# Performance work log

Hardware: AMD Instinct MI355X
Metric: run time of the kernel (lower is better)

The kernel has to match this reference:

```python
import jax, jax.numpy as jnp
import numpy as np

N = 50000   # num nodes
D = 64      # feature dim
R = 4       # num relations (len(adjs))
E = 800000  # edges per relation (avg degree 16)


def setup_inputs() -> dict:
    key = jax.random.key(0)
    k0, k1, k2, k3, k4 = jax.random.split(key, 5)
    x = jax.random.normal(k0, (N, D), dtype=jnp.float32)
    weight = jax.random.normal(k1, (R,), dtype=jnp.float32)        # scalar weight per relation
    edge_vals = jax.random.uniform(k2, (R, E), dtype=jnp.float32)  # nonzero values of adjs
    edge_rows = jax.random.randint(k3, (R, E), 0, N)               # COO row (destination) indices
    edge_cols = jax.random.randint(k4, (R, E), 0, N)               # COO col (source) indices
    return {"x": x, "weight": weight, "edge_vals": edge_vals,
            "edge_rows": edge_rows, "edge_cols": edge_cols, "idx": 1}


def reference(x, weight, edge_vals, edge_rows, edge_cols, idx):
    # spmm(adjs[idx], x): gather source features, scale by edge values, scatter-add to rows
    rows = edge_rows[idx]
    cols = edge_cols[idx]
    vals = edge_vals[idx]
    msgs = vals[:, None] * x[cols]                                  # [E, D]
    agg = jax.ops.segment_sum(msgs, rows, num_segments=N)           # [N, D]
    return weight[idx] * agg
```

## Files before the change

kernel.cpp:

```cpp
#include <hip/hip_runtime.h>


#define FEAT_D 64
#define BROWS 32
#define BSH 5
#define LCAP 48
#define OVFCAP 16384
#define EPB 4096
#define BBLOCK 512
#define EPT (EPB / BBLOCK)
#define GBLOCK 512

__global__ __launch_bounds__(BBLOCK) void build_kernel(
        const float* __restrict__ edge_vals,
        const int* __restrict__ edge_rows,
        const int* __restrict__ edge_cols,
        const int* __restrict__ idx_ptr,
        int* __restrict__ bktcnt,
        int2* __restrict__ pack,
        int* __restrict__ ovfcnt,
        int4* __restrict__ ovfbuf,
        int E, int NBKT, int cap) {
    extern __shared__ int lh[];
    const long long off = (long long)idx_ptr[0] * E;
    const int* rows = edge_rows + off;
    const int* cols = edge_cols + off;
    const float* vals = edge_vals + off;
    for (int k = threadIdx.x; k < NBKT; k += BBLOCK) lh[k] = 0;
    __syncthreads();
    const int s = blockIdx.x * EPB;
    const int e2 = min(s + EPB, E);
    int myrow[EPT];
#pragma unroll
    for (int k = 0; k < EPT; ++k) {
        const int g = s + threadIdx.x + k * BBLOCK;
        if (g < e2) {
            const int r = rows[g];
            myrow[k] = r;
            atomicAdd(&lh[r >> BSH], 1);
        }
    }
    __syncthreads();
    for (int k = threadIdx.x; k < NBKT; k += BBLOCK) {
        const int c = lh[k];
        if (c) lh[k] = atomicAdd(&bktcnt[k], c);
    }
    __syncthreads();
#pragma unroll
    for (int k = 0; k < EPT; ++k) {
        const int g = s + threadIdx.x + k * BBLOCK;
        if (g < e2) {
            const int r = myrow[k];
            const int b = r >> BSH;
            const int c = cols[g];
            const float v = vals[g];
            const int pos = atomicAdd(&lh[b], 1);
            if (pos < cap) {
                pack[(long long)b * cap + pos] =
                    make_int2((c << BSH) | (r & (BROWS - 1)), __float_as_int(v));
            } else {
                const int o = atomicAdd(ovfcnt, 1);
                if (o < OVFCAP) ovfbuf[o] = make_int4(r, c, __float_as_int(v), 0);
            }
        }
    }
}

__global__ __launch_bounds__(GBLOCK) void gather_kernel(
        const float* __restrict__ x,
        const float* __restrict__ weight,
        const int* __restrict__ idx_ptr,
        const int* __restrict__ bktcnt,
        const int2* __restrict__ pack,
        int* __restrict__ ovfcnt, int4* __restrict__ ovfbuf,
        float* __restrict__ out, int N, int cap) {
    __shared__ int2 slist[BROWS * LCAP];
    __shared__ int scur[BROWS];
    const int b = blockIdx.x;
    const int t = threadIdx.x;
    const int w = t >> 6;
    const int lane = t & 63;
    if (t < BROWS) scur[t] = 0;
    __syncthreads();
    const int cnt = min(bktcnt[b], cap);
    const long long* psrc = (const long long*)(pack + (long long)b * cap);
    for (int j = t; j < cnt; j += GBLOCK) {
        const long long raw = __builtin_nontemporal_load(psrc + j);
        const int2 rec = make_int2((int)(unsigned)raw, (int)(raw >> 32));
        const int rl = rec.x & (BROWS - 1);
        const int li = atomicAdd(&scur[rl], 1);
        if (li < LCAP) {
            slist[rl * LCAP + li] = rec;
        } else {
            const int o = atomicAdd(ovfcnt, 1);
            const int row = (b << BSH) | rl;
            if (o < OVFCAP) ovfbuf[o] = make_int4(row, rec.x >> BSH, rec.y, 0);
        }
    }
    __syncthreads();
    const float ws = weight[idx_ptr[0]];
    float acc0 = 0.f, acc1 = 0.f, acc2 = 0.f, acc3 = 0.f;
#define ROWACC(Q, ACC)                                                        \
    {                                                                         \
        const int rl = w * 4 + Q;                                             \
        const int n = min(scur[rl], LCAP);                                    \
        const int2* lp = slist + rl * LCAP;                                   \
        int j = 0;                                                            \
        for (; j + 4 <= n; j += 4) {                                          \
            const int2 r0 = lp[j], r1 = lp[j + 1], r2 = lp[j + 2],            \
                       r3 = lp[j + 3];                                        \
            const float x0 = x[(r0.x >> BSH) * FEAT_D + lane];                \
            const float x1 = x[(r1.x >> BSH) * FEAT_D + lane];                \
            const float x2 = x[(r2.x >> BSH) * FEAT_D + lane];                \
            const float x3 = x[(r3.x >> BSH) * FEAT_D + lane];                \
            ACC += __int_as_float(r0.y) * x0 + __int_as_float(r1.y) * x1 +    \
                   __int_as_float(r2.y) * x2 + __int_as_float(r3.y) * x3;     \
        }                                                                     \
        for (; j < n; ++j) {                                                  \
            const int2 r0 = lp[j];                                            \
            ACC += __int_as_float(r0.y) * x[(r0.x >> BSH) * FEAT_D + lane];   \
        }                                                                     \
    }
    ROWACC(0, acc0)
    ROWACC(1, acc1)
    ROWACC(2, acc2)
    ROWACC(3, acc3)
#undef ROWACC
    const int row0 = (b << BSH) + w * 4;
    if (row0 + 0 < N)
        __builtin_nontemporal_store(ws * acc0, &out[(long long)(row0 + 0) * FEAT_D + lane]);
    if (row0 + 1 < N)
        __builtin_nontemporal_store(ws * acc1, &out[(long long)(row0 + 1) * FEAT_D + lane]);
    if (row0 + 2 < N)
        __builtin_nontemporal_store(ws * acc2, &out[(long long)(row0 + 2) * FEAT_D + lane]);
    if (row0 + 3 < N)
        __builtin_nontemporal_store(ws * acc3, &out[(long long)(row0 + 3) * FEAT_D + lane]);
}

__global__ void fixup_kernel(const float* __restrict__ x,
                             const float* __restrict__ weight,
                             const int* __restrict__ idx_ptr,
                             const int* __restrict__ ovfcnt,
                             const int4* __restrict__ ovfbuf,
                             float* __restrict__ out) {
    const int n = min(*ovfcnt, OVFCAP);
    if (n == 0) return;
    const float ws = weight[idx_ptr[0]];
    const int gw = (int)((blockIdx.x * (long long)blockDim.x + threadIdx.x) >> 6);
    const int lane = threadIdx.x & 63;
    const int nw = (gridDim.x * blockDim.x) >> 6;
    for (int r = gw; r < n; r += nw) {
        const int4 rec = ovfbuf[r];
        atomicAdd(&out[(long long)rec.x * FEAT_D + lane],
                  ws * __int_as_float(rec.z) * x[(long long)rec.y * FEAT_D + lane]);
    }
}

__global__ void spmm_scatter_kernel(const float* __restrict__ x,
                                    const float* __restrict__ weight,
                                    const float* __restrict__ edge_vals,
                                    const int* __restrict__ edge_rows,
                                    const int* __restrict__ edge_cols,
                                    const int* __restrict__ idx_ptr,
                                    float* __restrict__ out,
                                    int E, long long work) {
    const int idx = idx_ptr[0];
    const float w = weight[idx];
    const long long rel_off = (long long)idx * E;
    long long t = (long long)blockIdx.x * blockDim.x + threadIdx.x;
    if (t >= work) return;
    const int e = (int)(t >> 4);
    const int q = (int)(t & 15);
    const int r = edge_rows[rel_off + e];
    const int c = edge_cols[rel_off + e];
    const float wv = w * edge_vals[rel_off + e];
    const float4 xv = *reinterpret_cast<const float4*>(x + (long long)c * FEAT_D + q * 4);
    float* op = out + (long long)r * FEAT_D + q * 4;
    atomicAdd(op + 0, wv * xv.x);
    atomicAdd(op + 1, wv * xv.y);
    atomicAdd(op + 2, wv * xv.z);
    atomicAdd(op + 3, wv * xv.w);
}

extern "C" void kernel_launch(void* const* d_in, const int* in_sizes, int n_in,
                              void* d_out, int out_size, void* d_ws, size_t ws_size,
                              hipStream_t stream) {
    const float* x         = (const float*)d_in[0];
    const float* weight    = (const float*)d_in[1];
    const float* edge_vals = (const float*)d_in[2];
    const int*   edge_rows = (const int*)d_in[3];
    const int*   edge_cols = (const int*)d_in[4];
    const int*   idx_ptr   = (const int*)d_in[5];
    float* out = (float*)d_out;

    const int R = in_sizes[1];
    const int E = in_sizes[2] / R;
    const int N = in_sizes[0] / FEAT_D;
    const int NBKT = (N + BROWS - 1) >> BSH;

    char* ws = (char*)d_ws;
    size_t o_bktcnt = 0;
    size_t o_ovfcnt = o_bktcnt + (size_t)NBKT * 4;
    size_t o_ovfbuf = ((o_ovfcnt + 4 + 15) / 16) * 16;
    size_t o_pack   = o_ovfbuf + (size_t)OVFCAP * 16;
    const size_t room = (ws_size > o_pack) ? (ws_size - o_pack) : 0;
    int cap = (int)(room / ((size_t)NBKT * 8));
    if (cap > 1024) cap = 1024;

    const long long meanload = (NBKT > 0) ? ((long long)E / NBKT) : 0;
    if (cap < 64 || cap < meanload + (meanload >> 3) + 16 || NBKT > 8192) {
        hipMemsetAsync(d_out, 0, (size_t)out_size * sizeof(float), stream);
        const long long work = (long long)E * 16;
        const int block = 256;
        const long long grid = (work + block - 1) / block;
        spmm_scatter_kernel<<<dim3((unsigned)grid), dim3(block), 0, stream>>>(
            x, weight, edge_vals, edge_rows, edge_cols, idx_ptr, out, E, work);
        return;
    }

    int*  bktcnt = (int*)(ws + o_bktcnt);
    int*  ovfcnt = (int*)(ws + o_ovfcnt);
    int4* ovfbuf = (int4*)(ws + o_ovfbuf);
    int2* pack   = (int2*)(ws + o_pack);

    hipMemsetAsync(bktcnt, 0, (size_t)NBKT * 4 + 4, stream);

    const int bgrid = (E + EPB - 1) / EPB;
    const size_t blds = (size_t)NBKT * 4;
    build_kernel<<<bgrid, BBLOCK, blds, stream>>>(edge_vals, edge_rows,
                                                  edge_cols, idx_ptr, bktcnt,
                                                  pack, ovfcnt, ovfbuf,
                                                  E, NBKT, cap);

    gather_kernel<<<NBKT, GBLOCK, 0, stream>>>(x, weight, idx_ptr, bktcnt,
                                               pack, ovfcnt, ovfbuf,
                                               out, N, cap);

    fixup_kernel<<<64, 256, 0, stream>>>(x, weight, idx_ptr, ovfcnt, ovfbuf, out);
}
```

Baseline: 138.8 us.

## Stage edges in LDS by bucket before coalesced global writes; widen buckets

The build kernel now counting-sorts each 4096-edge chunk by destination bucket in shared memory, using a block prefix scan, before writing. Each bucket's records can then go out as a contiguous run with one global atomic per bucket, instead of scattered per-edge writes. Buckets grow from 32 to 64 rows, so each gather wave handles 8 rows and the pack capacity and fallback thresholds are raised to match. In exchange, the build kernel uses far more static shared memory and loses occupancy, the gather grid halves, and a smaller workspace would push execution onto the slow scatter fallback.

```diff
diff --git a/kernel.cpp b/kernel.cpp
--- a/kernel.cpp
+++ b/kernel.cpp
@@ -2,9 +2,10 @@
 
 
 #define FEAT_D 64
-#define BROWS 32
-#define BSH 5
-#define LCAP 48
+#define BROWS 64
+#define BSH 6
+#define MAXBKT 1024
+#define LCAP 44
 #define OVFCAP 16384
 #define EPB 4096
 #define BBLOCK 512
@@ -21,47 +22,89 @@
         int* __restrict__ ovfcnt,
         int4* __restrict__ ovfbuf,
         int E, int NBKT, int cap) {
-    extern __shared__ int lh[];
+    __shared__ int2 stage[EPB];
+    __shared__ unsigned short sbkt[EPB];
+    __shared__ int lh[MAXBKT];
+    __shared__ int lofs[MAXBKT];
+    __shared__ int gbase[MAXBKT];
+    __shared__ int ssum[BBLOCK];
     const long long off = (long long)idx_ptr[0] * E;
     const int* rows = edge_rows + off;
     const int* cols = edge_cols + off;
     const float* vals = edge_vals + off;
-    for (int k = threadIdx.x; k < NBKT; k += BBLOCK) lh[k] = 0;
-    __syncthreads();
+    const int t = threadIdx.x;
     const int s = blockIdx.x * EPB;
     const int e2 = min(s + EPB, E);
-    int myrow[EPT];
+    const int cnt_total = e2 - s;
+
+    for (int k = t; k < NBKT; k += BBLOCK) lh[k] = 0;
+    __syncthreads();
+
+    int2 myrec[EPT];
+    int mybkt[EPT];
 #pragma unroll
     for (int k = 0; k < EPT; ++k) {
-        const int g = s + threadIdx.x + k * BBLOCK;
+        const int g = s + t + k * BBLOCK;
+        mybkt[k] = -1;
         if (g < e2) {
             const int r = rows[g];
-            myrow[k] = r;
-            atomicAdd(&lh[r >> BSH], 1);
-        }
-    }
-    __syncthreads();
-    for (int k = threadIdx.x; k < NBKT; k += BBLOCK) {
-        const int c = lh[k];
-        if (c) lh[k] = atomicAdd(&bktcnt[k], c);
-    }
-    __syncthreads();
-#pragma unroll
-    for (int k = 0; k < EPT; ++k) {
-        const int g = s + threadIdx.x + k * BBLOCK;
-        if (g < e2) {
-            const int r = myrow[k];
-            const int b = r >> BSH;
             const int c = cols[g];
             const float v = vals[g];
-            const int pos = atomicAdd(&lh[b], 1);
-            if (pos < cap) {
-                pack[(long long)b * cap + pos] =
-                    make_int2((c << BSH) | (r & (BROWS - 1)), __float_as_int(v));
-            } else {
-                const int o = atomicAdd(ovfcnt, 1);
-                if (o < OVFCAP) ovfbuf[o] = make_int4(r, c, __float_as_int(v), 0);
-            }
+            mybkt[k] = r >> BSH;
+            myrec[k] = make_int2((c << BSH) | (r & (BROWS - 1)), __float_as_int(v));
+            atomicAdd(&lh[mybkt[k]], 1);
+        }
+    }
+    __syncthreads();
+
+    const int i0 = 2 * t, i1 = 2 * t + 1;
+    const int a0 = (i0 < NBKT) ? lh[i0] : 0;
+    const int a1 = (i1 < NBKT) ? lh[i1] : 0;
+    ssum[t] = a0 + a1;
+    __syncthreads();
+    for (int d = 1; d < BBLOCK; d <<= 1) {
+        const int add = (t >= d) ? ssum[t - d] : 0;
+        __syncthreads();
+        ssum[t] += add;
+        __syncthreads();
+    }
+    const int exc = ssum[t] - (a0 + a1);
+    if (i0 < NBKT) lofs[i0] = exc;
+    if (i1 < NBKT) lofs[i1] = exc + a0;
+    __syncthreads();
+
+    for (int k = t; k < NBKT; k += BBLOCK) lh[k] = lofs[k];
+    __syncthreads();
+
+#pragma unroll
+    for (int k = 0; k < EPT; ++k) {
+        if (mybkt[k] >= 0) {
+            const int pos = atomicAdd(&lh[mybkt[k]], 1);
+            stage[pos] = myrec[k];
+            sbkt[pos] = (unsigned short)mybkt[k];
+        }
+    }
+    __syncthreads();
+
+    for (int k = t; k < NBKT; k += BBLOCK) {
+        const int c = lh[k] - lofs[k];
+        gbase[k] = (c > 0) ? atomicAdd(&bktcnt[k], c) : 0;
+    }
+    __syncthreads();
+
+    for (int p = t; p < cnt_total; p += BBLOCK) {
+        const int k = sbkt[p];
+        const int g = gbase[k] + (p - lofs[k]);
+        const int2 rec = stage[p];
+        if (g < cap) {
+            __builtin_nontemporal_store(
+                *(const long long*)&rec,
+                (long long*)(pack + (long long)k * cap + g));
+        } else {
+            const int o = atomicAdd(ovfcnt, 1);
+            if (o < OVFCAP)
+                ovfbuf[o] = make_int4((k << BSH) | (rec.x & (BROWS - 1)),
+                                      rec.x >> BSH, rec.y, 0);
         }
     }
 }
@@ -93,48 +136,43 @@
             slist[rl * LCAP + li] = rec;
         } else {
             const int o = atomicAdd(ovfcnt, 1);
-            const int row = (b << BSH) | rl;
-            if (o < OVFCAP) ovfbuf[o] = make_int4(row, rec.x >> BSH, rec.y, 0);
+            if (o < OVFCAP)
+                ovfbuf[o] = make_int4((b << BSH) | rl, rec.x >> BSH, rec.y, 0);
         }
     }
     __syncthreads();
     const float ws = weight[idx_ptr[0]];
-    float acc0 = 0.f, acc1 = 0.f, acc2 = 0.f, acc3 = 0.f;
-#define ROWACC(Q, ACC)                                                        \
-    {                                                                         \
-        const int rl = w * 4 + Q;                                             \
-        const int n = min(scur[rl], LCAP);                                    \
-        const int2* lp = slist + rl * LCAP;                                   \
-        int j = 0;                                                            \
-        for (; j + 4 <= n; j += 4) {                                          \
-            const int2 r0 = lp[j], r1 = lp[j + 1], r2 = lp[j + 2],            \
-                       r3 = lp[j + 3];                                        \
-            const float x0 = x[(r0.x >> BSH) * FEAT_D + lane];                \
-            const float x1 = x[(r1.x >> BSH) * FEAT_D + lane];                \
-            const float x2 = x[(r2.x >> BSH) * FEAT_D + lane];                \
-            const float x3 = x[(r3.x >> BSH) * FEAT_D + lane];                \
-            ACC += __int_as_float(r0.y) * x0 + __int_as_float(r1.y) * x1 +    \
-                   __int_as_float(r2.y) * x2 + __int_as_float(r3.y) * x3;     \
-        }                                                                     \
-        for (; j < n; ++j) {                                                  \
-            const int2 r0 = lp[j];                                            \
-            ACC += __int_as_float(r0.y) * x[(r0.x >> BSH) * FEAT_D + lane];   \
-        }                                                                     \
-    }
-    ROWACC(0, acc0)
-    ROWACC(1, acc1)
-    ROWACC(2, acc2)
-    ROWACC(3, acc3)
-#undef ROWACC
-    const int row0 = (b << BSH) + w * 4;
-    if (row0 + 0 < N)
-        __builtin_nontemporal_store(ws * acc0, &out[(long long)(row0 + 0) * FEAT_D + lane]);
-    if (row0 + 1 < N)
-        __builtin_nontemporal_store(ws * acc1, &out[(long long)(row0 + 1) * FEAT_D + lane]);
-    if (row0 + 2 < N)
-        __builtin_nontemporal_store(ws * acc2, &out[(long long)(row0 + 2) * FEAT_D + lane]);
-    if (row0 + 3 < N)
-        __builtin_nontemporal_store(ws * acc3, &out[(long long)(row0 + 3) * FEAT_D + lane]);
+    float acc[8];
+#pragma unroll
+    for (int q = 0; q < 8; ++q) acc[q] = 0.f;
+#pragma unroll
+    for (int q = 0; q < 8; ++q) {
+        const int rl = w * 8 + q;
+        const int n = min(scur[rl], LCAP);
+        const int2* lp = slist + rl * LCAP;
+        int j = 0;
+        for (; j + 4 <= n; j += 4) {
+            const int2 r0 = lp[j], r1 = lp[j + 1], r2 = lp[j + 2], r3 = lp[j + 3];
+            const float x0 = x[(r0.x >> BSH) * FEAT_D + lane];
+            const float x1 = x[(r1.x >> BSH) * FEAT_D + lane];
+            const float x2 = x[(r2.x >> BSH) * FEAT_D + lane];
+            const float x3 = x[(r3.x >> BSH) * FEAT_D + lane];
+            acc[q] += __int_as_float(r0.y) * x0 + __int_as_float(r1.y) * x1 +
+                      __int_as_float(r2.y) * x2 + __int_as_float(r3.y) * x3;
+        }
+        for (; j < n; ++j) {
+            const int2 r0 = lp[j];
+            acc[q] += __int_as_float(r0.y) * x[(r0.x >> BSH) * FEAT_D + lane];
+        }
+    }
+    const int row0 = (b << BSH) + w * 8;
+#pragma unroll
+    for (int q = 0; q < 8; ++q) {
+        const int row = row0 + q;
+        if (row < N)
+            __builtin_nontemporal_store(ws * acc[q],
+                                        &out[(long long)row * FEAT_D + lane]);
+    }
 }
 
 __global__ void fixup_kernel(const float* __restrict__ x,
@@ -205,10 +243,10 @@
     size_t o_pack   = o_ovfbuf + (size_t)OVFCAP * 16;
     const size_t room = (ws_size > o_pack) ? (ws_size - o_pack) : 0;
     int cap = (int)(room / ((size_t)NBKT * 8));
-    if (cap > 1024) cap = 1024;
+    if (cap > 2048) cap = 2048;
 
     const long long meanload = (NBKT > 0) ? ((long long)E / NBKT) : 0;
-    if (cap < 64 || cap < meanload + (meanload >> 3) + 16 || NBKT > 8192) {
+    if (cap < 128 || cap < meanload + (meanload >> 3) + 32 || NBKT > MAXBKT) {
         hipMemsetAsync(d_out, 0, (size_t)out_size * sizeof(float), stream);
         const long long work = (long long)E * 16;
         const int block = 256;
@@ -226,11 +264,10 @@
     hipMemsetAsync(bktcnt, 0, (size_t)NBKT * 4 + 4, stream);
 
     const int bgrid = (E + EPB - 1) / EPB;
-    const size_t blds = (size_t)NBKT * 4;
-    build_kernel<<<bgrid, BBLOCK, blds, stream>>>(edge_vals, edge_rows,
-                                                  edge_cols, idx_ptr, bktcnt,
-                                                  pack, ovfcnt, ovfbuf,
-                                                  E, NBKT, cap);
+    build_kernel<<<bgrid, BBLOCK, 0, stream>>>(edge_vals, edge_rows,
+                                               edge_cols, idx_ptr, bktcnt,
+                                               pack, ovfcnt, ovfbuf,
+                                               E, NBKT, cap);
 
     gather_kernel<<<NBKT, GBLOCK, 0, stream>>>(x, weight, idx_ptr, bktcnt,
                                                pack, ovfcnt, ovfbuf,
```

Measured after the change: 135.6 us. 2.4% less time.
